# Performance work log

Hardware: AMD Instinct MI355X
Metric: run time of the kernel (lower is better)

The kernel has to match this reference:

```python
import jax, jax.numpy as jnp
import numpy as np

BOUND = np.array([[-4.0, 4.0], [-4.0, 4.0], [-2.0, 2.0]], dtype=np.float32)
N_PTS = 1048576
PLANE_C = 3
PLANE_RES = [128, 256, 512, 1024]
N_LEVELS = 16
F_PER = 2
T = 2 ** 16  # hashmap size (log2_hashmap_size=16)
BASE_RES = 16
FINEST = int(float((BOUND[:, 1] - BOUND[:, 0]).max()) / 0.02)  # 400
_growth = np.exp(np.log(FINEST / BASE_RES) / (N_LEVELS - 1))
HASH_RES = np.floor(BASE_RES * _growth ** np.arange(N_LEVELS)).astype(np.float32)
PRIMES = jnp.array([1, 2654435761, 805459861], dtype=jnp.uint32)


def setup_inputs() -> dict:
    key = jax.random.key(0)
    ks = jax.random.split(key, 32)
    lo = jnp.asarray(BOUND[:, 0]); hi = jnp.asarray(BOUND[:, 1])
    inp = {}
    inp['p'] = jax.random.uniform(ks[0], (N_PTS, 3), dtype=jnp.float32) * (hi - lo) + lo
    i = 1
    for li, r in enumerate(PLANE_RES):
        for name in ('xy', 'xz', 'yz'):
            inp[f'plane_{name}_{li}'] = 0.1 * jax.random.normal(ks[i], (PLANE_C, r, r), dtype=jnp.float32)
            i += 1
    inp['hash_table'] = jax.random.uniform(ks[i], (N_LEVELS, T, F_PER), dtype=jnp.float32, minval=-1e-4, maxval=1e-4); i += 1

    def lin(k, fi, fo):
        s = 1.0 / np.sqrt(fi)
        k1, k2 = jax.random.split(k)
        return (jax.random.uniform(k1, (fi, fo), minval=-s, maxval=s, dtype=jnp.float32),
                jax.random.uniform(k2, (fo,), minval=-s, maxval=s, dtype=jnp.float32))

    c_in = 12 * PLANE_C + N_LEVELS * F_PER  # 68
    inp['W0'], inp['b0'] = lin(ks[i], c_in, 64); i += 1
    inp['W1'], inp['b1'] = lin(ks[i], 64, 64); i += 1
    inp['Wo'], inp['bo'] = lin(ks[i], 64, 33); i += 1  # 1 sdf + 32 geo_feat
    inp['Wc0'], inp['bc0'] = lin(ks[i], 12 * PLANE_C + 32, 64); i += 1
    inp['Wc1'], inp['bc1'] = lin(ks[i], 64, 32); i += 1
    inp['Wco'], inp['bco'] = lin(ks[i], 32, 3); i += 1
    return inp


def sample_plane(plane, u, v):
    """Bilinear grid_sample, align_corners=True, padding_mode='border'.
    plane: (C,H,W); u indexes W, v indexes H; u,v in [-1,1]. Returns (N,C)."""
    C, H, W = plane.shape
    x = jnp.clip((u + 1.0) * 0.5 * (W - 1), 0.0, W - 1)
    y = jnp.clip((v + 1.0) * 0.5 * (H - 1), 0.0, H - 1)
    x0 = jnp.floor(x); y0 = jnp.floor(y)
    wx = x - x0; wy = y - y0
    x0i = x0.astype(jnp.int32); y0i = y0.astype(jnp.int32)
    x1i = jnp.minimum(x0i + 1, W - 1); y1i = jnp.minimum(y0i + 1, H - 1)
    g = lambda yi, xi: plane[:, yi, xi]  # (C,N)
    out = (g(y0i, x0i) * ((1 - wy) * (1 - wx)) + g(y0i, x1i) * ((1 - wy) * wx)
           + g(y1i, x0i) * (wy * (1 - wx)) + g(y1i, x1i) * (wy * wx))
    return out.T


def hash_encode(p01, table):
    """Multi-res hash grid (instant-ngp style). p01: (N,3) in [0,1]; table: (L,T,F) -> (N, L*F)."""
    res = jnp.asarray(HASH_RES)  # (L,)

    def level(r, tab):
        x = p01 * r
        x0 = jnp.floor(x)
        w = x - x0
        xi = x0.astype(jnp.uint32)  # (N,3)
        feat = jnp.zeros((p01.shape[0], F_PER), dtype=table.dtype)
        for dz in (0, 1):
            for dy in (0, 1):
                for dx in (0, 1):
                    c = xi + jnp.array([dx, dy, dz], dtype=jnp.uint32)
                    h = c * PRIMES[None, :]
                    idx = ((h[:, 0] ^ h[:, 1] ^ h[:, 2]) % T).astype(jnp.int32)
                    wgt = ((w[:, 0] if dx else 1 - w[:, 0])
                           * (w[:, 1] if dy else 1 - w[:, 1])
                           * (w[:, 2] if dz else 1 - w[:, 2]))
                    feat = feat + tab[idx] * wgt[:, None]
        return feat  # (N,F)

    feats = jax.vmap(level, in_axes=(0, 0))(res, table)  # (L,N,F)
    return jnp.transpose(feats, (1, 0, 2)).reshape(p01.shape[0], N_LEVELS * F_PER)


def _forward(p, plane_xy_0, plane_xz_0, plane_yz_0, plane_xy_1, plane_xz_1, plane_yz_1,
             plane_xy_2, plane_xz_2, plane_yz_2, plane_xy_3, plane_xz_3, plane_yz_3,
             hash_table, W0, b0, W1, b1, Wo, bo, Wc0, bc0, Wc1, bc1, Wco, bco):
    bound = jnp.asarray(BOUND)
    p_nor = (p - bound[:, 0]) / (bound[:, 1] - bound[:, 0]) * 2.0 - 1.0  # normalize_3d_coordinate
    u, v, w = p_nor[:, 0], p_nor[:, 1], p_nor[:, 2]
    levels = [(plane_xy_0, plane_xz_0, plane_yz_0), (plane_xy_1, plane_xz_1, plane_yz_1),
              (plane_xy_2, plane_xz_2, plane_yz_2), (plane_xy_3, plane_xz_3, plane_yz_3)]
    feats = []
    for pxy, pxz, pyz in levels:
        feats += [sample_plane(pxy, u, v), sample_plane(pxz, u, w), sample_plane(pyz, v, w)]
    plane_feat = jnp.concatenate(feats, axis=-1)  # (N, 36)
    hfeat = hash_encode((p_nor + 1.0) * 0.5, hash_table)  # (N, 32)
    # SDF branch
    h = jnp.concatenate([plane_feat, hfeat], axis=-1)  # (N, 68)
    h = jax.nn.relu(h @ W0 + b0)
    h = jax.nn.relu(h @ W1 + b1)
    sf = jnp.tanh(h @ Wo + bo)
    sdf, geo_feat = sf[:, :1], sf[:, 1:]
    # RGB branch
    c = jnp.concatenate([geo_feat, plane_feat], axis=-1)  # (N, 68)
    c = jax.nn.relu(c @ Wc0 + bc0)
    c = jax.nn.relu(c @ Wc1 + bc1)
    rgb = jax.nn.sigmoid(c @ Wco + bco)
    return jnp.concatenate([rgb, sdf], axis=-1)  # (N, 4)


def reference(p, plane_xy_0, plane_xz_0, plane_yz_0, plane_xy_1, plane_xz_1, plane_yz_1,
              plane_xy_2, plane_xz_2, plane_yz_2, plane_xy_3, plane_xz_3, plane_yz_3,
              hash_table, W0, b0, W1, b1, Wo, bo, Wc0, bc0, Wc1, bc1, Wco, bco):
    return _forward(p, plane_xy_0, plane_xz_0, plane_yz_0, plane_xy_1, plane_xz_1, plane_yz_1,
                    plane_xy_2, plane_xz_2, plane_yz_2, plane_xy_3, plane_xz_3, plane_yz_3,
                    hash_table, W0, b0, W1, b1, Wo, bo, Wc0, bc0, Wc1, bc1, Wco, bco)
```

## Files before the change

kernel.cpp:

```cpp
#include <hip/hip_runtime.h>

#define NPTS 1048576
#define NBKT 262144

typedef short bhalf8 __attribute__((ext_vector_type(8)));
typedef _Float16 halfv8 __attribute__((ext_vector_type(8)));
typedef _Float16 halfv2 __attribute__((ext_vector_type(2)));
typedef float floatx4 __attribute__((ext_vector_type(4)));

#define WSZ 24320
#define FROWS 22
#define MLP_THREADS 1024
#define MLP_WAVES 16

#define PB_PLANES 16320
#define PB_HASH 4096
#define PB_HIST 4096

__device__ const float HRg[16] = {16.f, 19.f, 24.f, 30.f, 37.f, 46.f, 57.f, 71.f,
                                  89.f, 110.f, 136.f, 169.f, 210.f, 260.f, 322.f, 400.f};


__device__ __forceinline__ float my_tanh(float x) {
  float e = __expf(2.f * x);
  return 1.f - 2.f * __builtin_amdgcn_rcpf(e + 1.f);
}

__device__ __forceinline__ float my_sigmoid(float x) {
  return __builtin_amdgcn_rcpf(1.f + __expf(-x));
}

__device__ __forceinline__ unsigned short f2h(float v) {
  _Float16 h = (_Float16)v;
  unsigned short u;
  __builtin_memcpy(&u, &h, 2);
  return u;
}

__device__ __forceinline__ float h2f(unsigned short u) {
  _Float16 h;
  __builtin_memcpy(&h, &u, 2);
  return (float)h;
}

__device__ __forceinline__ float texch(uint2 t, int c) {
  unsigned short u = (c == 0) ? (unsigned short)(t.x & 0xffffu)
                   : (c == 1) ? (unsigned short)(t.x >> 16)
                              : (unsigned short)(t.y & 0xffffu);
  return h2f(u);
}

__device__ __forceinline__ unsigned mort6(unsigned x) {
  return (x & 1) | ((x & 2) << 2) | ((x & 4) << 4) |
         ((x & 8) << 6) | ((x & 16) << 8) | ((x & 32) << 10);
}

__device__ __forceinline__ unsigned morton_key(float px, float py, float pz) {
  float qx = (px + 4.f) * 0.125f, qy = (py + 4.f) * 0.125f, qz = (pz + 2.f) * 0.25f;
  unsigned kx = min(63, max(0, (int)(qx * 64.f)));
  unsigned ky = min(63, max(0, (int)(qy * 64.f)));
  unsigned kz = min(63, max(0, (int)(qz * 64.f)));
  return mort6(kx) | (mort6(ky) << 1) | (mort6(kz) << 2);
}

__device__ __forceinline__ unsigned hash_level(const unsigned* __restrict__ ht, int lv,
                                               float q0, float q1, float q2) {
  const float r = HRg[lv];
  float x0 = q0 * r, x1 = q1 * r, x2 = q2 * r;
  float f0 = floorf(x0), f1 = floorf(x1), f2 = floorf(x2);
  float w0 = x0 - f0, w1 = x1 - f1, w2 = x2 - f2;
  unsigned i0 = (unsigned)(int)f0, i1 = (unsigned)(int)f1, i2 = (unsigned)(int)f2;
  const unsigned* __restrict__ hb = ht + ((unsigned)lv << 16);
  unsigned tv[8];
#pragma unroll
  for (int dz = 0; dz < 2; ++dz)
#pragma unroll
    for (int dy = 0; dy < 2; ++dy)
#pragma unroll
      for (int dx = 0; dx < 2; ++dx) {
        unsigned h = (i0 + dx) ^ ((i1 + dy) * 2654435761u) ^ ((i2 + dz) * 805459861u);
        tv[dz * 4 + dy * 2 + dx] = hb[h & 65535u];
      }
  halfv2 acc2 = {(_Float16)0.f, (_Float16)0.f};
#pragma unroll
  for (int c = 0; c < 8; ++c) {
    const int dx = c & 1, dy = (c >> 1) & 1, dz = c >> 2;
    float wgt = (dx ? w0 : 1.f - w0) * (dy ? w1 : 1.f - w1) * (dz ? w2 : 1.f - w2);
    halfv2 th;
    __builtin_memcpy(&th, &tv[c], 4);
    _Float16 wh = (_Float16)wgt;
    halfv2 w2v = {wh, wh};
    acc2 = th * w2v + acc2;
  }
  unsigned res;
  __builtin_memcpy(&res, &acc2, 4);
  return res;
}


struct PrepParams {
  const float* psrc[12];
  ushort4* pdst[12];
  const float* hash;
  unsigned* hashb;
  const float* p;
  unsigned* hist;
};

__global__ __launch_bounds__(256) void prep_kernel(PrepParams P) {
  const int b = blockIdx.x;
  if (b < PB_PLANES) {
    const int CUM[13] = {0, 16384, 32768, 49152, 114688, 180224, 245760,
                         507904, 770048, 1032192, 2080768, 3129344, 4177920};
    const int RESL[12] = {128, 128, 128, 256, 256, 256, 512, 512, 512, 1024, 1024, 1024};
    const int s = b << 8;
    int pi = 0;
#pragma unroll
    for (int i = 1; i < 12; ++i)
      if (s >= CUM[i]) pi = i;
    const int li = s + threadIdx.x - CUM[pi];
    const int R = RESL[pi];
    const int n = R * R;
    const float* __restrict__ src = P.psrc[pi];
    ushort4 t;
    t.x = f2h(src[li]);
    t.y = f2h(src[n + li]);
    t.z = f2h(src[2 * n + li]);
    t.w = 0;
    P.pdst[pi][li] = t;
  } else if (b < PB_PLANES + PB_HASH) {
    const int i = ((b - PB_PLANES) << 8) + threadIdx.x;
    float2 v = *(const float2*)(P.hash + (size_t)i * 2);
    P.hashb[i] = (unsigned)f2h(v.x) | ((unsigned)f2h(v.y) << 16);
  } else {
    const int i = ((b - PB_PLANES - PB_HASH) << 8) + threadIdx.x;
    const float* pp = P.p + (size_t)i * 3;
    unsigned k = morton_key(pp[0], pp[1], pp[2]);
    atomicAdd(&P.hist[k], 1u);
  }
}


__global__ __launch_bounds__(256) void scan1_kernel(const unsigned* __restrict__ hist,
                                                    unsigned* __restrict__ partial) {
  __shared__ unsigned s[256];
  const int b = blockIdx.x, t = threadIdx.x;
  uint4 v = ((const uint4*)(hist + b * 1024))[t];
  s[t] = v.x + v.y + v.z + v.w;
  __syncthreads();
  for (int d = 128; d > 0; d >>= 1) {
    if (t < d) s[t] += s[t + d];
    __syncthreads();
  }
  if (t == 0) partial[b] = s[0];
}

__global__ __launch_bounds__(256) void scan23_kernel(const unsigned* __restrict__ hist,
                                                     const unsigned* __restrict__ partial,
                                                     unsigned* __restrict__ cursor) {
  __shared__ unsigned sp[256];
  __shared__ unsigned s2[256];
  const int b = blockIdx.x, t = threadIdx.x;
  sp[t] = partial[t];
  __syncthreads();
  for (int d = 1; d < 256; d <<= 1) {
    unsigned v = (t >= d) ? sp[t - d] : 0u;
    __syncthreads();
    sp[t] += v;
    __syncthreads();
  }
  const unsigned base = (b == 0) ? 0u : sp[b - 1];

  uint4 v = ((const uint4*)(hist + b * 1024))[t];
  unsigned sum = v.x + v.y + v.z + v.w;
  s2[t] = sum;
  __syncthreads();
  for (int d = 1; d < 256; d <<= 1) {
    unsigned x = (t >= d) ? s2[t - d] : 0u;
    __syncthreads();
    s2[t] += x;
    __syncthreads();
  }
  unsigned off = base + s2[t] - sum;
  uint4 c;
  c.x = off;
  c.y = off + v.x;
  c.z = off + v.x + v.y;
  c.w = off + v.x + v.y + v.z;
  ((uint4*)(cursor + b * 1024))[t] = c;
}

__global__ __launch_bounds__(256) void scatter_kernel(const float* __restrict__ p,
                                                      unsigned* __restrict__ cursor,
                                                      float4* __restrict__ qs) {
  int i = blockIdx.x * 256 + threadIdx.x;
  const float* pp = p + (size_t)i * 3;
  const float px = pp[0], py = pp[1], pz = pp[2];
  unsigned k = morton_key(px, py, pz);
  unsigned slot = atomicAdd(&cursor[k], 1u);
  float4 q;
  q.x = (px + 4.f) * 0.125f;
  q.y = (py + 4.f) * 0.125f;
  q.z = (pz + 2.f) * 0.25f;
  q.w = __uint_as_float((unsigned)i);
  qs[slot] = q;
}


__global__ __launch_bounds__(256) void repack_plane(const float* __restrict__ src,
                                                    ushort4* __restrict__ dst, int R) {
  int i = blockIdx.x * 256 + threadIdx.x;
  int n = R * R;
  if (i >= n) return;
  ushort4 t;
  t.x = f2h(src[i]);
  t.y = f2h(src[n + i]);
  t.z = f2h(src[2 * n + i]);
  t.w = 0;
  dst[i] = t;
}


__device__ __forceinline__ void sample3i(const uint2* __restrict__ pl,
                                         float a, float b, int R, float* f) {
  const float Rm1 = (float)(R - 1);
  float x = fminf(fmaxf((a + 1.f) * 0.5f * Rm1, 0.f), Rm1);
  float y = fminf(fmaxf((b + 1.f) * 0.5f * Rm1, 0.f), Rm1);
  float x0f = floorf(x), y0f = floorf(y);
  float wx = x - x0f, wy = y - y0f;
  int x0 = (int)x0f, y0 = (int)y0f;
  int x1 = min(x0 + 1, R - 1), y1 = min(y0 + 1, R - 1);
  float w00 = (1.f - wy) * (1.f - wx);
  float w01 = (1.f - wy) * wx;
  float w10 = wy * (1.f - wx);
  float w11 = wy * wx;
  uint2 t00 = pl[y0 * R + x0];
  uint2 t01 = pl[y0 * R + x1];
  uint2 t10 = pl[y1 * R + x0];
  uint2 t11 = pl[y1 * R + x1];
#pragma unroll
  for (int c = 0; c < 3; ++c) {
    f[c] = texch(t00, c) * w00 + texch(t01, c) * w01 +
           texch(t10, c) * w10 + texch(t11, c) * w11;
  }
}

__device__ __forceinline__ void sample3f(const float* __restrict__ pl,
                                         float a, float b, int R, float* f) {
  const float Rm1 = (float)(R - 1);
  float x = fminf(fmaxf((a + 1.f) * 0.5f * Rm1, 0.f), Rm1);
  float y = fminf(fmaxf((b + 1.f) * 0.5f * Rm1, 0.f), Rm1);
  float x0f = floorf(x), y0f = floorf(y);
  float wx = x - x0f, wy = y - y0f;
  int x0 = (int)x0f, y0 = (int)y0f;
  int x1 = min(x0 + 1, R - 1), y1 = min(y0 + 1, R - 1);
  float w00 = (1.f - wy) * (1.f - wx);
  float w01 = (1.f - wy) * wx;
  float w10 = wy * (1.f - wx);
  float w11 = wy * wx;
  int i00 = y0 * R + x0, i01 = y0 * R + x1;
  int i10 = y1 * R + x0, i11 = y1 * R + x1;
  const int R2 = R * R;
#pragma unroll
  for (int c = 0; c < 3; ++c) {
    const float* base = pl + c * R2;
    f[c] = base[i00] * w00 + base[i01] * w01 + base[i10] * w10 + base[i11] * w11;
  }
}


struct FeatParams {
  const float4* qs;
  const uint2* pli[12];
  unsigned* fbuf;
};

__global__ __launch_bounds__(256) void feat_kernel(FeatParams P) {
  int bid = blockIdx.x;
  bid = (bid & 7) * (NPTS / 256 / 8) + (bid >> 3);
  const int tid = bid * 256 + threadIdx.x;

  float4 q4 = P.qs[tid];
  const float u = 2.f * q4.x - 1.f;
  const float v = 2.f * q4.y - 1.f;
  const float w = 2.f * q4.z - 1.f;

  float pf[36];
  {
    const int RES[4] = {128, 256, 512, 1024};
#pragma unroll
    for (int li = 0; li < 4; ++li) {
      sample3i(P.pli[li * 3 + 0], u, v, RES[li], &pf[li * 9 + 0]);
      sample3i(P.pli[li * 3 + 1], u, w, RES[li], &pf[li * 9 + 3]);
      sample3i(P.pli[li * 3 + 2], v, w, RES[li], &pf[li * 9 + 6]);
    }
  }
  unsigned* __restrict__ F = P.fbuf;
#pragma unroll
  for (int kk = 0; kk < 18; ++kk) {
    unsigned pk = (unsigned)f2h(pf[2 * kk]) | ((unsigned)f2h(pf[2 * kk + 1]) << 16);
    F[(size_t)kk * NPTS + tid] = pk;
  }
  F[(size_t)18 * NPTS + tid] = __float_as_uint(q4.x);
  F[(size_t)19 * NPTS + tid] = __float_as_uint(q4.y);
  F[(size_t)20 * NPTS + tid] = __float_as_uint(q4.z);
  F[(size_t)21 * NPTS + tid] = __float_as_uint(q4.w);
}


struct MlpWParams {
  const unsigned* fbuf;
  const unsigned* hashb;
  const float* W0; const float* b0;
  const float* W1; const float* b1;
  const float* Wo; const float* bo;
  const float* Wc0; const float* bc0;
  const float* Wc1; const float* bc1;
  const float* Wco; const float* bco;
  float* out;
};

__device__ __forceinline__ void stage_w(const float* __restrict__ src, int K, int Nsrc,
                                        int STR, int NPAD, int OFF, short* Wlds, int tid) {
  const int total = NPAD * STR;
  for (int idx = tid; idx < total; idx += MLP_THREADS) {
    int c = idx / STR;
    int k = idx - c * STR;
    float val = (k < K && c < Nsrc) ? src[k * Nsrc + c] : 0.f;
    Wlds[OFF + idx] = (short)f2h(val);
  }
}

__device__ __forceinline__ void stage_b(const float* __restrict__ src, int Nsrc, int NPAD,
                                        int BOFF, float* Blds, int tid) {
  for (int j = tid; j < NPAD; j += MLP_THREADS) Blds[BOFF + j] = (j < Nsrc) ? src[j] : 0.f;
}

__device__ __forceinline__ halfv8 as_h8(bhalf8 s) {
  halfv8 h;
  __builtin_memcpy(&h, &s, 16);
  return h;
}

__device__ __forceinline__ halfv8 ldA(const unsigned* __restrict__ fbuf, int pt,
                                      int kkBase, int kkLim) {
  bhalf8 r;
#pragma unroll
  for (int j = 0; j < 4; ++j) {
    const int kk = kkBase + j;
    unsigned d = 0u;
    if (kk < kkLim) d = fbuf[(size_t)kk * NPTS + pt];
    r[2 * j] = (short)(d & 0xffffu);
    r[2 * j + 1] = (short)(d >> 16);
  }
  return as_h8(r);
}

__device__ __forceinline__ halfv8 frag4(unsigned d0, unsigned d1, unsigned d2, unsigned d3) {
  bhalf8 r;
  r[0] = (short)(d0 & 0xffffu); r[1] = (short)(d0 >> 16);
  r[2] = (short)(d1 & 0xffffu); r[3] = (short)(d1 >> 16);
  r[4] = (short)(d2 & 0xffffu); r[5] = (short)(d2 >> 16);
  r[6] = (short)(d3 & 0xffffu); r[7] = (short)(d3 >> 16);
  return as_h8(r);
}

__device__ __forceinline__ halfv8 ldS(const short* scr, int rowl, int grp, int s) {
  return *(const halfv8*)&scr[rowl * 72 + 32 * s + 8 * grp];
}

template <int NT, int KS, int OFF, int STR>
__device__ __forceinline__ void mlayer(const halfv8 (&af)[KS], floatx4 (&acc)[NT],
                                       const short* Wlds, int rowl, int grp) {
#pragma unroll
  for (int n = 0; n < NT; ++n) {
    floatx4 a{};
#pragma unroll
    for (int s = 0; s < KS; ++s) {
      const int wo = OFF + (16 * n + rowl) * STR + 32 * s + 8 * grp;
      const halfv8 wA = *(const halfv8*)&Wlds[wo];
      a = __builtin_amdgcn_mfma_f32_16x16x32_f16(wA, af[s], a, 0, 0, 0);
    }
    acc[n] = a;
  }
}

template <int NT>
__device__ __forceinline__ void relu_wr(const floatx4 (&acc)[NT], const float* Blds,
                                        int boff, short* scr, int rowl, int grp) {
#pragma unroll
  for (int n = 0; n < NT; ++n) {
    const int cbase = 16 * n + 4 * grp;
    short4 v4;
    float v0 = fmaxf(acc[n][0] + Blds[boff + cbase + 0], 0.f);
    float v1 = fmaxf(acc[n][1] + Blds[boff + cbase + 1], 0.f);
    float v2 = fmaxf(acc[n][2] + Blds[boff + cbase + 2], 0.f);
    float v3 = fmaxf(acc[n][3] + Blds[boff + cbase + 3], 0.f);
    v4.x = (short)f2h(v0);
    v4.y = (short)f2h(v1);
    v4.z = (short)f2h(v2);
    v4.w = (short)f2h(v3);
    *(short4*)&scr[rowl * 72 + cbase] = v4;
  }
}

__device__ __forceinline__ void tanh_wr(const floatx4 (&acc)[3], const float* Blds,
                                        short* scr, float* ost, int rowl, int grp) {
#pragma unroll
  for (int n = 0; n < 3; ++n) {
#pragma unroll
    for (int r = 0; r < 4; ++r) {
      const int c = 16 * n + 4 * grp + r;
      float v = my_tanh(acc[n][r] + Blds[128 + c]);
      if (c == 0) ost[rowl * 4 + 3] = v;
      if (c >= 1 && c <= 32) scr[rowl * 72 + c - 1] = (short)f2h(v);
    }
  }
}

__global__ __launch_bounds__(MLP_THREADS) void mlp_mfma(MlpWParams P) {
  __shared__ short Wlds[WSZ];
  __shared__ float Blds[288];
  __shared__ short Scr[MLP_WAVES * 16 * 72];
  __shared__ float Ost[MLP_WAVES][16][4];

  const int tid = threadIdx.x;

  stage_w(P.W0,  68, 64, 104, 64,     0, Wlds, tid);
  stage_w(P.W1,  64, 64,  72, 64,  6656, Wlds, tid);
  stage_w(P.Wo,  64, 33,  72, 48, 11264, Wlds, tid);
  stage_w(P.Wc0, 68, 64, 104, 64, 14720, Wlds, tid);
  stage_w(P.Wc1, 64, 32,  72, 32, 21376, Wlds, tid);
  stage_w(P.Wco, 32,  3,  40, 16, 23680, Wlds, tid);
  stage_b(P.b0,  64, 64,   0, Blds, tid);
  stage_b(P.b1,  64, 64,  64, Blds, tid);
  stage_b(P.bo,  33, 48, 128, Blds, tid);
  stage_b(P.bc0, 64, 64, 176, Blds, tid);
  stage_b(P.bc1, 32, 32, 240, Blds, tid);
  stage_b(P.bco,  3, 16, 272, Blds, tid);
  __syncthreads();

  const int wave = tid >> 6, lane = tid & 63;
  const int rowl = lane & 15, grp = lane >> 4;
  short* scr0 = &Scr[wave * 16 * 72];
  float* ost0 = &Ost[wave][0][0];

  const int lv0 = (grp == 0) ? 0 : (4 * grp - 2);

  int bid = blockIdx.x;
  bid = (bid & 7) * 64 + (bid >> 3);

  for (int t = 0; t < 8; ++t) {
    const int wbase = ((bid * 8 + t) * MLP_WAVES + wave) * 16;
    const int ptA = wbase + rowl;

    halfv8 af0A;
    unsigned pA16, pA17;
    unsigned pid;

    {
      const unsigned* __restrict__ F = P.fbuf;
      float qA0 = __uint_as_float(F[(size_t)18 * NPTS + ptA]);
      float qA1 = __uint_as_float(F[(size_t)19 * NPTS + ptA]);
      float qA2 = __uint_as_float(F[(size_t)20 * NPTS + ptA]);
      pid = F[(size_t)21 * NPTS + ptA];

      unsigned hA0, hA1, hA2, hA3;
      {
        const int l0 = lv0, l1 = lv0 + 1;
        const int l2 = (grp == 0) ? 14 : (lv0 + 2);
        const int l3 = (grp == 0) ? 15 : (lv0 + 3);
        hA0 = hash_level(P.hashb, l0, qA0, qA1, qA2);
        hA1 = hash_level(P.hashb, l1, qA0, qA1, qA2);
        hA2 = hash_level(P.hashb, l2, qA0, qA1, qA2);
        hA3 = hash_level(P.hashb, l3, qA0, qA1, qA2);
      }

      pA16 = F[(size_t)16 * NPTS + ptA];
      pA17 = F[(size_t)17 * NPTS + ptA];

      halfv8 s1A = (grp == 0) ? frag4(pA16, pA17, hA0, hA1) : frag4(hA0, hA1, hA2, hA3);
      halfv8 s2A = (grp == 0) ? frag4(hA2, hA3, 0u, 0u) : frag4(0u, 0u, 0u, 0u);

      af0A = ldA(P.fbuf, ptA, 4 * grp, 18);
      halfv8 afA[3] = {af0A, s1A, s2A};
      floatx4 accA[4];
      mlayer<4, 3, 0, 104>(afA, accA, Wlds, rowl, grp);
      relu_wr<4>(accA, Blds, 0, scr0, rowl, grp);
    }
    {
      halfv8 afA[2] = {ldS(scr0, rowl, grp, 0), ldS(scr0, rowl, grp, 1)};
      floatx4 accA[4];
      mlayer<4, 2, 6656, 72>(afA, accA, Wlds, rowl, grp);
      relu_wr<4>(accA, Blds, 64, scr0, rowl, grp);
    }
    {
      halfv8 afA[2] = {ldS(scr0, rowl, grp, 0), ldS(scr0, rowl, grp, 1)};
      floatx4 accA[3];
      mlayer<3, 2, 11264, 72>(afA, accA, Wlds, rowl, grp);
      tanh_wr(accA, Blds, scr0, ost0, rowl, grp);
    }
    {
      halfv8 s2 = (grp == 0) ? frag4(pA16, pA17, 0u, 0u) : frag4(0u, 0u, 0u, 0u);
      halfv8 afA[3] = {ldS(scr0, rowl, grp, 0), af0A, s2};
      floatx4 accA[4];
      mlayer<4, 3, 14720, 104>(afA, accA, Wlds, rowl, grp);
      relu_wr<4>(accA, Blds, 176, scr0, rowl, grp);
    }
    {
      halfv8 afA[2] = {ldS(scr0, rowl, grp, 0), ldS(scr0, rowl, grp, 1)};
      floatx4 accA[2];
      mlayer<2, 2, 21376, 72>(afA, accA, Wlds, rowl, grp);
      relu_wr<2>(accA, Blds, 240, scr0, rowl, grp);
    }
    {
      halfv8 afA[1] = {ldS(scr0, rowl, grp, 0)};
      floatx4 accA[1];
      mlayer<1, 1, 23680, 40>(afA, accA, Wlds, rowl, grp);
#pragma unroll
      for (int r = 0; r < 4; ++r) {
        const int c = 4 * grp + r;
        if (c < 3) {
          float vA = my_sigmoid(accA[0][r] + Blds[272 + c]);
          ost0[rowl * 4 + c] = vA;
        }
      }
    }

    if (lane < 16) {
      float4 o = *(float4*)&Ost[wave][lane][0];
      ((float4*)P.out)[pid] = o;
    }
  }
}


struct DecParams {
  const float* p;
  const float* pl[12];
  const uint2* pli[12];
  const float* hash;
  const float* W0; const float* b0;
  const float* W1; const float* b1;
  const float* Wo; const float* bo;
  const float* Wc0; const float* bc0;
  const float* Wc1; const float* bc1;
  const float* Wco; const float* bco;
  float* out;
};

template <bool ILV>
__global__ __launch_bounds__(256) void dec_kernel(DecParams P) {
  const int tid = blockIdx.x * 256 + threadIdx.x;

  const float* __restrict__ pp = P.p + (size_t)tid * 3;
  const float px = pp[0], py = pp[1], pz = pp[2];

  const float u = (px + 4.f) * 0.25f - 1.f;
  const float v = (py + 4.f) * 0.25f - 1.f;
  const float w = (pz + 2.f) * 0.5f - 1.f;

  float feat[68];
  {
    const int RES[4] = {128, 256, 512, 1024};
#pragma unroll
    for (int li = 0; li < 4; ++li) {
      if (ILV) {
        sample3i(P.pli[li * 3 + 0], u, v, RES[li], &feat[li * 9 + 0]);
        sample3i(P.pli[li * 3 + 1], u, w, RES[li], &feat[li * 9 + 3]);
        sample3i(P.pli[li * 3 + 2], v, w, RES[li], &feat[li * 9 + 6]);
      } else {
        sample3f(P.pl[li * 3 + 0], u, v, RES[li], &feat[li * 9 + 0]);
        sample3f(P.pl[li * 3 + 1], u, w, RES[li], &feat[li * 9 + 3]);
        sample3f(P.pl[li * 3 + 2], v, w, RES[li], &feat[li * 9 + 6]);
      }
    }
  }

  {
    const float q0 = (px + 4.f) * 0.125f;
    const float q1 = (py + 4.f) * 0.125f;
    const float q2 = (pz + 2.f) * 0.25f;
    const float* __restrict__ ht = P.hash;
#pragma unroll
    for (int l = 0; l < 16; ++l) {
      const float r = HRg[l];
      float x0 = q0 * r, x1 = q1 * r, x2 = q2 * r;
      float f0 = floorf(x0), f1 = floorf(x1), f2 = floorf(x2);
      float w0 = x0 - f0, w1 = x1 - f1, w2 = x2 - f2;
      unsigned i0 = (unsigned)(int)f0, i1 = (unsigned)(int)f1, i2 = (unsigned)(int)f2;
      float a0 = 0.f, a1 = 0.f;
#pragma unroll
      for (int dz = 0; dz < 2; ++dz)
#pragma unroll
        for (int dy = 0; dy < 2; ++dy)
#pragma unroll
          for (int dx = 0; dx < 2; ++dx) {
            unsigned h = (i0 + dx) ^ ((i1 + dy) * 2654435761u) ^ ((i2 + dz) * 805459861u);
            unsigned idx = h & 65535u;
            const float2 tv = *(const float2*)(ht + (((unsigned)l << 16) + idx) * 2);
            float wgt = (dx ? w0 : 1.f - w0) * (dy ? w1 : 1.f - w1) * (dz ? w2 : 1.f - w2);
            a0 = fmaf(tv.x, wgt, a0);
            a1 = fmaf(tv.y, wgt, a1);
          }
      feat[36 + l * 2] = a0;
      feat[36 + l * 2 + 1] = a1;
    }
  }

  float acc[64];
#pragma unroll
  for (int j = 0; j < 64; ++j) acc[j] = P.b0[j];
#pragma unroll
  for (int i = 0; i < 68; ++i) {
    const float a = feat[i];
    const float* wr = P.W0 + i * 64;
#pragma unroll
    for (int j = 0; j < 64; ++j) acc[j] = fmaf(a, wr[j], acc[j]);
  }
  float hid[64];
#pragma unroll
  for (int j = 0; j < 64; ++j) hid[j] = fmaxf(acc[j], 0.f);

#pragma unroll
  for (int j = 0; j < 64; ++j) acc[j] = P.b1[j];
#pragma unroll
  for (int i = 0; i < 64; ++i) {
    const float a = hid[i];
    const float* wr = P.W1 + i * 64;
#pragma unroll
    for (int j = 0; j < 64; ++j) acc[j] = fmaf(a, wr[j], acc[j]);
  }
#pragma unroll
  for (int j = 0; j < 64; ++j) hid[j] = fmaxf(acc[j], 0.f);

  float so[33];
#pragma unroll
  for (int j = 0; j < 33; ++j) so[j] = P.bo[j];
#pragma unroll
  for (int i = 0; i < 64; ++i) {
    const float a = hid[i];
    const float* wr = P.Wo + i * 33;
#pragma unroll
    for (int j = 0; j < 33; ++j) so[j] = fmaf(a, wr[j], so[j]);
  }
  const float sdf = my_tanh(so[0]);
  float geo[32];
#pragma unroll
  for (int j = 0; j < 32; ++j) geo[j] = my_tanh(so[j + 1]);

#pragma unroll
  for (int j = 0; j < 64; ++j) acc[j] = P.bc0[j];
#pragma unroll
  for (int i = 0; i < 32; ++i) {
    const float a = geo[i];
    const float* wr = P.Wc0 + i * 64;
#pragma unroll
    for (int j = 0; j < 64; ++j) acc[j] = fmaf(a, wr[j], acc[j]);
  }
#pragma unroll
  for (int i = 0; i < 36; ++i) {
    const float a = feat[i];
    const float* wr = P.Wc0 + (32 + i) * 64;
#pragma unroll
    for (int j = 0; j < 64; ++j) acc[j] = fmaf(a, wr[j], acc[j]);
  }
#pragma unroll
  for (int j = 0; j < 64; ++j) hid[j] = fmaxf(acc[j], 0.f);

  float c1[32];
#pragma unroll
  for (int j = 0; j < 32; ++j) c1[j] = P.bc1[j];
#pragma unroll
  for (int i = 0; i < 64; ++i) {
    const float a = hid[i];
    const float* wr = P.Wc1 + i * 32;
#pragma unroll
    for (int j = 0; j < 32; ++j) c1[j] = fmaf(a, wr[j], c1[j]);
  }

  float r0 = P.bco[0], r1 = P.bco[1], r2 = P.bco[2];
#pragma unroll
  for (int i = 0; i < 32; ++i) {
    const float a = fmaxf(c1[i], 0.f);
    r0 = fmaf(a, P.Wco[i * 3 + 0], r0);
    r1 = fmaf(a, P.Wco[i * 3 + 1], r1);
    r2 = fmaf(a, P.Wco[i * 3 + 2], r2);
  }

  float4 o;
  o.x = my_sigmoid(r0);
  o.y = my_sigmoid(r1);
  o.z = my_sigmoid(r2);
  o.w = sdf;
  ((float4*)P.out)[tid] = o;
}


extern "C" void kernel_launch(void* const* d_in, const int* in_sizes, int n_in,
                              void* d_out, int out_size, void* d_ws, size_t ws_size,
                              hipStream_t stream) {
  const int RES[4] = {128, 256, 512, 1024};
  const size_t planes_bytes = (size_t)4177920 * 8;
  const size_t hash_bytes = (size_t)16 * 65536 * 4;
  const size_t feat_bytes = (size_t)FROWS * NPTS * 4;
  const size_t qs_bytes = (size_t)NPTS * 16;
  const size_t hist_bytes = (size_t)NBKT * 4;
  const size_t need_sort = planes_bytes + hash_bytes + feat_bytes + qs_bytes +
                           2 * hist_bytes + 4096;
  const size_t need_mid = planes_bytes + 64;

  char* wsp = (char*)d_ws;
  const float* p = (const float*)d_in[0];

  if (ws_size >= need_sort) {
    size_t off = 0;
    PrepParams PP;
    PP.p = p;
    PP.hash = (const float*)d_in[13];
    const uint2* pli[12];
    for (int i = 0; i < 12; ++i) {
      int R = RES[i / 3];
      PP.psrc[i] = (const float*)d_in[1 + i];
      PP.pdst[i] = (ushort4*)(wsp + off);
      pli[i] = (const uint2*)(wsp + off);
      off += (size_t)R * R * 8;
    }
    unsigned* hashb = (unsigned*)(wsp + off);
    PP.hashb = hashb;
    off += hash_bytes;
    unsigned* fbuf = (unsigned*)(wsp + off);
    off += feat_bytes;
    float4* qs = (float4*)(wsp + off);
    off += qs_bytes;
    unsigned* hist = (unsigned*)(wsp + off);
    off += hist_bytes;
    unsigned* cursor = (unsigned*)(wsp + off);
    off += hist_bytes;
    unsigned* partial = (unsigned*)(wsp + off);
    off += 2048;
    PP.hist = hist;

    hipMemsetAsync(hist, 0, hist_bytes, stream);
    prep_kernel<<<PB_PLANES + PB_HASH + PB_HIST, 256, 0, stream>>>(PP);
    scan1_kernel<<<256, 256, 0, stream>>>(hist, partial);
    scan23_kernel<<<256, 256, 0, stream>>>(hist, partial, cursor);
    scatter_kernel<<<NPTS / 256, 256, 0, stream>>>(p, cursor, qs);

    FeatParams FP;
    FP.qs = qs;
    for (int i = 0; i < 12; ++i) FP.pli[i] = pli[i];
    FP.fbuf = fbuf;
    feat_kernel<<<NPTS / 256, 256, 0, stream>>>(FP);

    MlpWParams MP;
    MP.fbuf = fbuf;
    MP.hashb = hashb;
    MP.W0 = (const float*)d_in[14]; MP.b0 = (const float*)d_in[15];
    MP.W1 = (const float*)d_in[16]; MP.b1 = (const float*)d_in[17];
    MP.Wo = (const float*)d_in[18]; MP.bo = (const float*)d_in[19];
    MP.Wc0 = (const float*)d_in[20]; MP.bc0 = (const float*)d_in[21];
    MP.Wc1 = (const float*)d_in[22]; MP.bc1 = (const float*)d_in[23];
    MP.Wco = (const float*)d_in[24]; MP.bco = (const float*)d_in[25];
    MP.out = (float*)d_out;
    mlp_mfma<<<512, MLP_THREADS, 0, stream>>>(MP);
    return;
  }

  DecParams P;
  P.p = p;
  for (int i = 0; i < 12; ++i) P.pl[i] = (const float*)d_in[1 + i];
  P.hash = (const float*)d_in[13];
  P.W0  = (const float*)d_in[14]; P.b0  = (const float*)d_in[15];
  P.W1  = (const float*)d_in[16]; P.b1  = (const float*)d_in[17];
  P.Wo  = (const float*)d_in[18]; P.bo  = (const float*)d_in[19];
  P.Wc0 = (const float*)d_in[20]; P.bc0 = (const float*)d_in[21];
  P.Wc1 = (const float*)d_in[22]; P.bc1 = (const float*)d_in[23];
  P.Wco = (const float*)d_in[24]; P.bco = (const float*)d_in[25];
  P.out = (float*)d_out;

  if (ws_size >= need_mid) {
    size_t off = 0;
    for (int i = 0; i < 12; ++i) {
      int R = RES[i / 3];
      int n = R * R;
      P.pli[i] = (const uint2*)(wsp + off);
      repack_plane<<<(n + 255) / 256, 256, 0, stream>>>(
          (const float*)d_in[1 + i], (ushort4*)(wsp + off), R);
      off += (size_t)n * 8;
    }
    dec_kernel<true><<<NPTS / 256, 256, 0, stream>>>(P);
  } else {
    for (int i = 0; i < 12; ++i) P.pli[i] = nullptr;
    dec_kernel<false><<<NPTS / 256, 256, 0, stream>>>(P);
  }
}
```

Before: 377.4 us.

## Move small MLP weight matrices from LDS to pre-converted global fp16 buffer

Wo, Wc1 and Wco are now converted to fp16 once in the prep kernel and written to a workspace buffer, so the MLP kernel reads them directly from global memory (through cache) instead of staging them in LDS. This cuts the LDS footprint of the MLP kernel, which, together with a launch-bounds occupancy hint, is meant to let more workgroups reside per CU and to shorten per-block staging. The cost is that those weight fragments now come from global/L2 loads inside the inner MFMA loop, with higher latency than LDS reads.

New measurement: 467.2 us. 1.24x slower.

```diff
diff --git a/kernel.cpp b/kernel.cpp
--- a/kernel.cpp
+++ b/kernel.cpp
@@ -8,13 +8,18 @@
 typedef _Float16 halfv2 __attribute__((ext_vector_type(2)));
 typedef float floatx4 __attribute__((ext_vector_type(4)));
 
-#define WSZ 24320
+#define WLDS_SZ 17920
+#define GW_WO 0
+#define GW_WC1 3456
+#define GW_WCO 5760
+#define GW_TOTAL 6400
 #define FROWS 22
 #define MLP_THREADS 1024
 #define MLP_WAVES 16
 
 #define PB_PLANES 16320
 #define PB_HASH 4096
+#define PB_W 25
 #define PB_HIST 4096
 
 __device__ const float HRg[16] = {16.f, 19.f, 24.f, 30.f, 37.f, 46.f, 57.f, 71.f,
@@ -103,6 +108,10 @@
   ushort4* pdst[12];
   const float* hash;
   unsigned* hashb;
+  const float* Wo;
+  const float* Wc1;
+  const float* Wco;
+  short* gw;
   const float* p;
   unsigned* hist;
 };
@@ -132,8 +141,24 @@
     const int i = ((b - PB_PLANES) << 8) + threadIdx.x;
     float2 v = *(const float2*)(P.hash + (size_t)i * 2);
     P.hashb[i] = (unsigned)f2h(v.x) | ((unsigned)f2h(v.y) << 16);
+  } else if (b < PB_PLANES + PB_HASH + PB_W) {
+    const int i = ((b - PB_PLANES - PB_HASH) << 8) + threadIdx.x;
+    float val = 0.f;
+    if (i < GW_WC1) {
+      int c = i / 72, k = i - c * 72;
+      val = (k < 64 && c < 33) ? P.Wo[k * 33 + c] : 0.f;
+    } else if (i < GW_WCO) {
+      int j = i - GW_WC1;
+      int c = j / 72, k = j - c * 72;
+      val = (k < 64 && c < 32) ? P.Wc1[k * 32 + c] : 0.f;
+    } else {
+      int j = i - GW_WCO;
+      int c = j / 40, k = j - c * 40;
+      val = (k < 32 && c < 3) ? P.Wco[k * 3 + c] : 0.f;
+    }
+    P.gw[i] = (short)f2h(val);
   } else {
-    const int i = ((b - PB_PLANES - PB_HASH) << 8) + threadIdx.x;
+    const int i = ((b - PB_PLANES - PB_HASH - PB_W) << 8) + threadIdx.x;
     const float* pp = P.p + (size_t)i * 3;
     unsigned k = morton_key(pp[0], pp[1], pp[2]);
     atomicAdd(&P.hist[k], 1u);
@@ -311,12 +336,13 @@
 struct MlpWParams {
   const unsigned* fbuf;
   const unsigned* hashb;
+  const short* gw;
   const float* W0; const float* b0;
   const float* W1; const float* b1;
-  const float* Wo; const float* bo;
+  const float* bo;
   const float* Wc0; const float* bc0;
-  const float* Wc1; const float* bc1;
-  const float* Wco; const float* bco;
+  const float* bc1;
+  const float* bco;
   float* out;
 };
 
@@ -379,6 +405,22 @@
     for (int s = 0; s < KS; ++s) {
       const int wo = OFF + (16 * n + rowl) * STR + 32 * s + 8 * grp;
       const halfv8 wA = *(const halfv8*)&Wlds[wo];
+      a = __builtin_amdgcn_mfma_f32_16x16x32_f16(wA, af[s], a, 0, 0, 0);
+    }
+    acc[n] = a;
+  }
+}
+
+template <int NT, int KS, int OFF, int STR>
+__device__ __forceinline__ void mlayerG(const halfv8 (&af)[KS], floatx4 (&acc)[NT],
+                                        const short* __restrict__ gw, int rowl, int grp) {
+#pragma unroll
+  for (int n = 0; n < NT; ++n) {
+    floatx4 a{};
+#pragma unroll
+    for (int s = 0; s < KS; ++s) {
+      const int wo = OFF + (16 * n + rowl) * STR + 32 * s + 8 * grp;
+      const halfv8 wA = *(const halfv8*)&gw[wo];
       a = __builtin_amdgcn_mfma_f32_16x16x32_f16(wA, af[s], a, 0, 0, 0);
     }
     acc[n] = a;
@@ -418,8 +460,8 @@
   }
 }
 
-__global__ __launch_bounds__(MLP_THREADS) void mlp_mfma(MlpWParams P) {
-  __shared__ short Wlds[WSZ];
+__global__ __launch_bounds__(MLP_THREADS, 8) void mlp_mfma(MlpWParams P) {
+  __shared__ short Wlds[WLDS_SZ];
   __shared__ float Blds[288];
   __shared__ short Scr[MLP_WAVES * 16 * 72];
   __shared__ float Ost[MLP_WAVES][16][4];
@@ -428,10 +470,7 @@
 
   stage_w(P.W0,  68, 64, 104, 64,     0, Wlds, tid);
   stage_w(P.W1,  64, 64,  72, 64,  6656, Wlds, tid);
-  stage_w(P.Wo,  64, 33,  72, 48, 11264, Wlds, tid);
-  stage_w(P.Wc0, 68, 64, 104, 64, 14720, Wlds, tid);
-  stage_w(P.Wc1, 64, 32,  72, 32, 21376, Wlds, tid);
-  stage_w(P.Wco, 32,  3,  40, 16, 23680, Wlds, tid);
+  stage_w(P.Wc0, 68, 64, 104, 64, 11264, Wlds, tid);
   stage_b(P.b0,  64, 64,   0, Blds, tid);
   stage_b(P.b1,  64, 64,  64, Blds, tid);
   stage_b(P.bo,  33, 48, 128, Blds, tid);
@@ -444,6 +483,7 @@
   const int rowl = lane & 15, grp = lane >> 4;
   short* scr0 = &Scr[wave * 16 * 72];
   float* ost0 = &Ost[wave][0][0];
+  const short* __restrict__ gw = P.gw;
 
   const int lv0 = (grp == 0) ? 0 : (4 * grp - 2);
 
@@ -497,26 +537,26 @@
     {
       halfv8 afA[2] = {ldS(scr0, rowl, grp, 0), ldS(scr0, rowl, grp, 1)};
       floatx4 accA[3];
-      mlayer<3, 2, 11264, 72>(afA, accA, Wlds, rowl, grp);
+      mlayerG<3, 2, GW_WO, 72>(afA, accA, gw, rowl, grp);
       tanh_wr(accA, Blds, scr0, ost0, rowl, grp);
     }
     {
       halfv8 s2 = (grp == 0) ? frag4(pA16, pA17, 0u, 0u) : frag4(0u, 0u, 0u, 0u);
       halfv8 afA[3] = {ldS(scr0, rowl, grp, 0), af0A, s2};
       floatx4 accA[4];
-      mlayer<4, 3, 14720, 104>(afA, accA, Wlds, rowl, grp);
+      mlayer<4, 3, 11264, 104>(afA, accA, Wlds, rowl, grp);
       relu_wr<4>(accA, Blds, 176, scr0, rowl, grp);
     }
     {
       halfv8 afA[2] = {ldS(scr0, rowl, grp, 0), ldS(scr0, rowl, grp, 1)};
       floatx4 accA[2];
-      mlayer<2, 2, 21376, 72>(afA, accA, Wlds, rowl, grp);
+      mlayerG<2, 2, GW_WC1, 72>(afA, accA, gw, rowl, grp);
       relu_wr<2>(accA, Blds, 240, scr0, rowl, grp);
     }
     {
       halfv8 afA[1] = {ldS(scr0, rowl, grp, 0)};
       floatx4 accA[1];
-      mlayer<1, 1, 23680, 40>(afA, accA, Wlds, rowl, grp);
+      mlayerG<1, 1, GW_WCO, 40>(afA, accA, gw, rowl, grp);
 #pragma unroll
       for (int r = 0; r < 4; ++r) {
         const int c = 4 * grp + r;
@@ -703,10 +743,11 @@
   const int RES[4] = {128, 256, 512, 1024};
   const size_t planes_bytes = (size_t)4177920 * 8;
   const size_t hash_bytes = (size_t)16 * 65536 * 4;
+  const size_t gw_bytes = 16384;
   const size_t feat_bytes = (size_t)FROWS * NPTS * 4;
   const size_t qs_bytes = (size_t)NPTS * 16;
   const size_t hist_bytes = (size_t)NBKT * 4;
-  const size_t need_sort = planes_bytes + hash_bytes + feat_bytes + qs_bytes +
+  const size_t need_sort = planes_bytes + hash_bytes + gw_bytes + feat_bytes + qs_bytes +
                            2 * hist_bytes + 4096;
   const size_t need_mid = planes_bytes + 64;
 
@@ -718,6 +759,9 @@
     PrepParams PP;
     PP.p = p;
     PP.hash = (const float*)d_in[13];
+    PP.Wo = (const float*)d_in[18];
+    PP.Wc1 = (const float*)d_in[22];
+    PP.Wco = (const float*)d_in[24];
     const uint2* pli[12];
     for (int i = 0; i < 12; ++i) {
       int R = RES[i / 3];
@@ -729,6 +773,9 @@
     unsigned* hashb = (unsigned*)(wsp + off);
     PP.hashb = hashb;
     off += hash_bytes;
+    short* gw = (short*)(wsp + off);
+    PP.gw = gw;
+    off += gw_bytes;
     unsigned* fbuf = (unsigned*)(wsp + off);
     off += feat_bytes;
     float4* qs = (float4*)(wsp + off);
@@ -742,7 +789,7 @@
     PP.hist = hist;
 
     hipMemsetAsync(hist, 0, hist_bytes, stream);
-    prep_kernel<<<PB_PLANES + PB_HASH + PB_HIST, 256, 0, stream>>>(PP);
+    prep_kernel<<<PB_PLANES + PB_HASH + PB_W + PB_HIST, 256, 0, stream>>>(PP);
     scan1_kernel<<<256, 256, 0, stream>>>(hist, partial);
     scan23_kernel<<<256, 256, 0, stream>>>(hist, partial, cursor);
     scatter_kernel<<<NPTS / 256, 256, 0, stream>>>(p, cursor, qs);
@@ -756,12 +803,13 @@
     MlpWParams MP;
     MP.fbuf = fbuf;
     MP.hashb = hashb;
+    MP.gw = gw;
     MP.W0 = (const float*)d_in[14]; MP.b0 = (const float*)d_in[15];
     MP.W1 = (const float*)d_in[16]; MP.b1 = (const float*)d_in[17];
-    MP.Wo = (const float*)d_in[18]; MP.bo = (const float*)d_in[19];
+    MP.bo = (const float*)d_in[19];
     MP.Wc0 = (const float*)d_in[20]; MP.bc0 = (const float*)d_in[21];
-    MP.Wc1 = (const float*)d_in[22]; MP.bc1 = (const float*)d_in[23];
-    MP.Wco = (const float*)d_in[24]; MP.bco = (const float*)d_in[25];
+    MP.bc1 = (const float*)d_in[23];
+    MP.bco = (const float*)d_in[25];
     MP.out = (float*)d_out;
     mlp_mfma<<<512, MLP_THREADS, 0, stream>>>(MP);
     return;
```
